# Performance work log

Measured on AMD Instinct MI355X. Metric: run time of the kernel, lower is better.

Reference implementation:

```python
import math
import jax, jax.numpy as jnp
import numpy as np
from jax import lax

SAMPLE_RATE = 16000
BLOCK_SIZE = 64
B = 524288


def setup_inputs() -> dict:
    key = jax.random.key(0)
    k1, k2, k3 = jax.random.split(key, 3)
    fm_params = jax.random.uniform(k1, (B, 1, 6), dtype=jnp.float32)
    # realistic fundamentals in [50, 400) Hz; module clamps to >=1 anyway
    f0_hz = 50.0 + 350.0 * jax.random.uniform(k2, (B, 1), dtype=jnp.float32)
    phase_state = jax.random.uniform(k3, (B, 4), dtype=jnp.float32)
    return {"fm_params": fm_params, "f0_hz": f0_hz, "phase_state": phase_state}


def reference(fm_params, f0_hz, phase_state):
    # T == 1 (module requirement), so squeeze the frame dim everywhere.
    dtype = fm_params.dtype
    two_pi = 2.0 * math.pi

    f0 = jnp.clip(f0_hz[:, 0], 1.0, None)            # [B]
    p = fm_params[:, 0, :]                            # [B, 6]
    # parameter mappings (op1 mod depth p[:,0] is unused, as in the original)
    r1 = 0.25 + p[:, 1] * 15.75
    fb1 = p[:, 2] * 0.95
    d2 = p[:, 3] * 10.0
    r2 = 0.25 + p[:, 4] * 15.75
    fb2 = p[:, 5] * 0.95

    inc1 = two_pi * f0 * r1 / SAMPLE_RATE             # [B]
    inc2 = two_pi * f0 * r2 / SAMPLE_RATE

    start1 = phase_state[:, 0]                        # frame start phases
    start2 = phase_state[:, 1]
    last1_0 = phase_state[:, 2]                       # feedback buffers
    last2_0 = phase_state[:, 3]

    offsets = jnp.arange(BLOCK_SIZE, dtype=dtype)     # [S]
    # per-sample phases, scanned over the sample axis: [S, B]
    phase1 = start1[None, :] + offsets[:, None] * inc1[None, :]
    phase2 = start2[None, :] + offsets[:, None] * inc2[None, :]

    def step(carry, ph):
        l1, l2 = carry
        ph1, ph2 = ph
        o1 = jnp.sin(ph1 + fb1 * l1)                  # op1 with self-feedback
        o2 = jnp.sin(ph2 + d2 * o1 + fb2 * l2)        # op2 carrier, FM'd by op1
        return (o1, o2), o2

    (l1f, l2f), samples = lax.scan(step, (last1_0, last2_0), (phase1, phase2))
    audio = samples.T                                 # [B, S]

    rms = jnp.sqrt(jnp.mean(audio * audio, axis=-1, keepdims=True) + 1e-5)
    audio = audio / rms

    phase_end = jnp.stack(
        [
            (start1 + BLOCK_SIZE * inc1) % two_pi,
            (start2 + BLOCK_SIZE * inc2) % two_pi,
            l1f,
            l2f,
        ],
        axis=-1,
    )                                                 # [B, 4]
    return audio, phase_end
```

## Files before the change

### kernel.cpp

```cpp
#include <hip/hip_runtime.h>

#define NBLOCK 64
#define TPB 256
#define CHV 16
#define LDSTR 68

__device__ __forceinline__ float fast_sinf(float x) {
    float kf = rintf(x * 0.63661977236758134f);
    int   q  = (int)kf;
    float r = fmaf(kf, -1.5707963705062866f, x);
    r = fmaf(kf, 4.3711390001862171e-8f, r);
    float z = r * r;
    float s = fmaf(z, fmaf(z, -1.9515295891e-4f, 8.3321608736e-3f), -1.6666654611e-1f);
    float sinr = fmaf(z * r, s, r);
    float c = fmaf(z, fmaf(z, 2.4433157118e-5f, -1.3887316255e-3f), 4.1666645683e-2f);
    float cosr = fmaf(z, fmaf(z, c, -0.5f), 1.0f);
    float res = (q & 1) ? cosr : sinr;
    return (q & 2) ? -res : res;
}

__device__ __forceinline__ float mod_two_pi(float x) {
    const float Y = 6.2831853071795864769f;
    float kf = floorf(__fdiv_rn(x, Y));
    float m = fmaf(-kf, Y, x);
    if (m < 0.0f)  { kf -= 1.0f; m = fmaf(-kf, Y, x); }
    if (m >= Y)    { kf += 1.0f; m = fmaf(-kf, Y, x); }
    return m;
}

__global__ __launch_bounds__(TPB)
void fm_synth_kernel(const float* __restrict__ fm_params,
                     const float* __restrict__ f0_hz,
                     const float* __restrict__ phase_state,
                     float* __restrict__ out, int nv)
{
    __shared__ float lds[4 * CHV * LDSTR];

    int tid  = threadIdx.x;
    int lane = tid & 63;
    int wv   = tid >> 6;
    int blockBase = blockIdx.x * TPB;
    int b   = blockBase + tid;
    int bc  = min(b, nv - 1);
    bool live = (b < nv);

    const float2* fm2 = (const float2*)fm_params;
    float2 p01 = fm2[bc * 3 + 0];
    float2 p23 = fm2[bc * 3 + 1];
    float2 p45 = fm2[bc * 3 + 2];
    float  f0  = fmaxf(f0_hz[bc], 1.0f);
    float4 st  = ((const float4*)phase_state)[bc];

    const float TWO_PI = 6.2831853071795864769f;
    float r1  = __fadd_rn(0.25f, __fmul_rn(p01.y, 15.75f));
    float fb1 = __fmul_rn(p23.x, 0.95f);
    float d2  = __fmul_rn(p23.y, 10.0f);
    float r2  = __fadd_rn(0.25f, __fmul_rn(p45.x, 15.75f));
    float fb2 = __fmul_rn(p45.y, 0.95f);
    float inc1 = __fdiv_rn(__fmul_rn(__fmul_rn(TWO_PI, f0), r1), 16000.0f);
    float inc2 = __fdiv_rn(__fmul_rn(__fmul_rn(TWO_PI, f0), r2), 16000.0f);

    float start1 = st.x, start2 = st.y;
    float l1 = st.z, l2 = st.w;

    float smp[NBLOCK];
#pragma unroll
    for (int t = 0; t < NBLOCK; ++t) {
        float tf  = (float)t;
        float ph1 = tf * inc1 + start1;
        float ph2 = tf * inc2 + start2;
        float o1 = fast_sinf(ph1 + fb1 * l1);
        float o2 = fast_sinf(ph2 + d2 * o1 + fb2 * l2);
        l1 = o1;
        l2 = o2;
        smp[t] = o2;
    }

    float ss = 0.0f;
#pragma unroll
    for (int t = 0; t < NBLOCK; ++t) ss = fmaf(smp[t], smp[t], ss);
    float inv = 1.0f / sqrtf(ss * 0.015625f + 1e-5f);
#pragma unroll
    for (int t = 0; t < NBLOCK; ++t) smp[t] *= inv;

    float x1 = __fadd_rn(start1, __fmul_rn(64.0f, inc1));
    float x2 = __fadd_rn(start2, __fmul_rn(64.0f, inc2));
    float4 pe;
    pe.x = mod_two_pi(x1);
    pe.y = mod_two_pi(x2);
    pe.z = l1;
    pe.w = l2;
    if (live)
        ((float4*)(out + (size_t)nv * NBLOCK))[b] = pe;

    float4* out4 = (float4*)out;
    float* slab = &lds[wv * (CHV * LDSTR)];
    int lg = lane >> 4;
    int vi = lane & 15;
#pragma unroll
    for (int g = 0; g < 4; ++g) {
        if (lg == g) {
            float* slot = &slab[vi * LDSTR];
#pragma unroll
            for (int i = 0; i < 16; ++i) {
                float4 v4;
                v4.x = smp[4 * i + 0];
                v4.y = smp[4 * i + 1];
                v4.z = smp[4 * i + 2];
                v4.w = smp[4 * i + 3];
                *(float4*)&slot[4 * i] = v4;
            }
        }
        int vbase = blockBase + wv * 64 + g * CHV;
        size_t gb4 = (size_t)vbase * 16;
#pragma unroll
        for (int j = 0; j < 4; ++j) {
            int f    = j * 64 + lane;
            int voff = f >> 4;
            float4 val = *(const float4*)&slab[voff * LDSTR + 4 * (f & 15)];
            if (vbase + voff < nv)
                out4[gb4 + f] = val;
        }
    }
}

extern "C" void kernel_launch(void* const* d_in, const int* in_sizes, int n_in,
                              void* d_out, int out_size, void* d_ws, size_t ws_size,
                              hipStream_t stream) {
    const float* fm_params   = (const float*)d_in[0];
    const float* f0_hz       = (const float*)d_in[1];
    const float* phase_state = (const float*)d_in[2];
    float* out = (float*)d_out;
    int nv = in_sizes[1];
    int grid = (nv + TPB - 1) / TPB;
    fm_synth_kernel<<<grid, TPB, 0, stream>>>(fm_params, f0_hz, phase_state, out, nv);
}
```

Baseline: 169.4 us.

## Pack synthesized samples as fp16 in registers and LDS, fuse RMS accumulation

```diff
diff --git a/kernel.cpp b/kernel.cpp
--- a/kernel.cpp
+++ b/kernel.cpp
@@ -2,8 +2,10 @@
 
 #define NBLOCK 64
 #define TPB 256
-#define CHV 16
-#define LDSTR 68
+#define ROWU 36
+
+typedef __fp16 half2_t __attribute__((ext_vector_type(2)));
+union PK { half2_t h2; unsigned int u; };
 
 __device__ __forceinline__ float fast_sinf(float x) {
     float kf = rintf(x * 0.63661977236758134f);
@@ -28,13 +30,13 @@
     return m;
 }
 
-__global__ __launch_bounds__(TPB)
+__global__ __launch_bounds__(TPB, 6)
 void fm_synth_kernel(const float* __restrict__ fm_params,
                      const float* __restrict__ f0_hz,
                      const float* __restrict__ phase_state,
                      float* __restrict__ out, int nv)
 {
-    __shared__ float lds[4 * CHV * LDSTR];
+    __shared__ unsigned int lds[4 * 32 * ROWU];
 
     int tid  = threadIdx.x;
     int lane = tid & 63;
@@ -63,7 +65,9 @@
     float start1 = st.x, start2 = st.y;
     float l1 = st.z, l2 = st.w;
 
-    float smp[NBLOCK];
+    unsigned int smph[32];
+    float ss = 0.0f;
+    float prev = 0.0f;
 #pragma unroll
     for (int t = 0; t < NBLOCK; ++t) {
         float tf  = (float)t;
@@ -73,15 +77,15 @@
         float o2 = fast_sinf(ph2 + d2 * o1 + fb2 * l2);
         l1 = o1;
         l2 = o2;
-        smp[t] = o2;
+        ss = fmaf(o2, o2, ss);
+        if (t & 1) {
+            PK pk; pk.h2 = __builtin_amdgcn_cvt_pkrtz(prev, o2);
+            smph[t >> 1] = pk.u;
+        } else {
+            prev = o2;
+        }
     }
-
-    float ss = 0.0f;
-#pragma unroll
-    for (int t = 0; t < NBLOCK; ++t) ss = fmaf(smp[t], smp[t], ss);
     float inv = 1.0f / sqrtf(ss * 0.015625f + 1e-5f);
-#pragma unroll
-    for (int t = 0; t < NBLOCK; ++t) smp[t] *= inv;
 
     float x1 = __fadd_rn(start1, __fmul_rn(64.0f, inc1));
     float x2 = __fadd_rn(start2, __fmul_rn(64.0f, inc2));
@@ -94,30 +98,42 @@
         ((float4*)(out + (size_t)nv * NBLOCK))[b] = pe;
 
     float4* out4 = (float4*)out;
-    float* slab = &lds[wv * (CHV * LDSTR)];
-    int lg = lane >> 4;
-    int vi = lane & 15;
+    unsigned int* slab = &lds[wv * (32 * ROWU)];
+    int grp = lane >> 5;
+    int row = lane & 31;
 #pragma unroll
-    for (int g = 0; g < 4; ++g) {
-        if (lg == g) {
-            float* slot = &slab[vi * LDSTR];
+    for (int c = 0; c < 2; ++c) {
+        if (grp == c) {
+            unsigned int* slot = &slab[row * ROWU];
 #pragma unroll
-            for (int i = 0; i < 16; ++i) {
-                float4 v4;
-                v4.x = smp[4 * i + 0];
-                v4.y = smp[4 * i + 1];
-                v4.z = smp[4 * i + 2];
-                v4.w = smp[4 * i + 3];
-                *(float4*)&slot[4 * i] = v4;
+            for (int i = 0; i < 8; ++i) {
+                uint4 w;
+                w.x = smph[4 * i + 0];
+                w.y = smph[4 * i + 1];
+                w.z = smph[4 * i + 2];
+                w.w = smph[4 * i + 3];
+                *(uint4*)&slot[4 * i] = w;
             }
+            slot[32] = __float_as_uint(inv);
         }
-        int vbase = blockBase + wv * 64 + g * CHV;
+        int vbase = blockBase + wv * 64 + c * 32;
         size_t gb4 = (size_t)vbase * 16;
 #pragma unroll
-        for (int j = 0; j < 4; ++j) {
+        for (int j = 0; j < 8; ++j) {
             int f    = j * 64 + lane;
             int voff = f >> 4;
-            float4 val = *(const float4*)&slab[voff * LDSTR + 4 * (f & 15)];
+            int p    = f & 15;
+            const unsigned int* rp = &slab[voff * ROWU + 2 * p];
+            unsigned int u0 = rp[0];
+            unsigned int u1 = rp[1];
+            float vinv = __uint_as_float(slab[voff * ROWU + 32]);
+            PK a; a.u = u0;
+            PK q; q.u = u1;
+            float4 val;
+            val.x = (float)a.h2.x * vinv;
+            val.y = (float)a.h2.y * vinv;
+            val.z = (float)q.h2.x * vinv;
+            val.w = (float)q.h2.y * vinv;
             if (vbase + voff < nv)
                 out4[gb4 + f] = val;
         }
```

Measured after the change: 180.4 us. 6.5% more time.
